# Kernel tuning notes

Measured on AMD Instinct MI355X. Metric: run time of the kernel, lower is better.

Reference implementation:

```python
import jax, jax.numpy as jnp
import numpy as np

B, N, C_IN, C_OUT, K, D_EMB = 32, 4096, 64, 64, 2, 16


def setup_inputs() -> dict:
    key = jax.random.key(0)
    ks = jax.random.split(key, 7)
    x = jax.random.normal(ks[0], (B, N, C_IN), jnp.float32)
    node_embeddings = jax.random.normal(ks[1], (N, D_EMB), jnp.float32)
    weights_pool = jax.random.normal(ks[2], (D_EMB, K, C_IN, C_OUT), jnp.float32) * 0.1
    bias_pool = jax.random.normal(ks[3], (D_EMB, C_OUT), jnp.float32) * 0.1
    lin_w = jax.random.normal(ks[4], (C_OUT, C_IN), jnp.float32) * 0.1
    lin_b = jax.random.normal(ks[5], (C_OUT,), jnp.float32) * 0.1
    adj = jax.random.uniform(ks[6], (N, N), jnp.float32)
    return dict(x=x, node_embeddings=node_embeddings, weights_pool=weights_pool,
                bias_pool=bias_pool, lin_w=lin_w, lin_b=lin_b, adj=adj)


def _sym_norm_adj(W):
    # W + 0.5*I, then D^{-1/2} W D^{-1/2} with D = diag(rowsum)
    n = W.shape[0]
    W = W + 0.5 * jnp.eye(n, dtype=W.dtype)
    sd = jnp.sqrt(1.0 / jnp.sum(W, axis=1))
    return sd[:, None] * W * sd[None, :]


def reference(x, node_embeddings, weights_pool, bias_pool, lin_w, lin_b, adj):
    n = node_embeddings.shape[0]
    # adaptive adjacency: softmax(relu(E E^T)) over neighbors
    supports_dyn = jax.nn.softmax(jax.nn.relu(node_embeddings @ node_embeddings.T), axis=1)
    supports = jnp.stack([jnp.eye(n, dtype=x.dtype), supports_dyn], axis=0)  # [K=2, N, N]
    # node-adaptive weights/bias generated from embeddings
    weights = jnp.einsum('nd,dkio->nkio', node_embeddings, weights_pool)  # [N,K,Cin,Cout]
    bias = node_embeddings @ bias_pool  # [N, Cout]
    # multi-hop aggregation + per-node conv
    x_g = jnp.einsum('knm,bmc->bnkc', supports, x)  # [B,N,K,Cin]
    x_gconv = jnp.einsum('bnki,nkio->bno', x_g, weights) + bias[None]  # [B,N,Cout]
    # static branch: init applies F.softmax(dim=1) to sym-normed adj, forward re-softmaxes dim=-1
    A = jax.nn.softmax(jax.nn.softmax(_sym_norm_adj(adj), axis=1), axis=-1)
    # einsum 'nm,bmc->bmc' == scale node m by sum_n A[n,m]
    scale = jnp.sum(A, axis=0)  # [N]
    x_static = (scale[None, :, None] * x) @ lin_w.T + lin_b  # [B,N,Cout]
    return x_gconv + jax.nn.sigmoid(x_static) * x_static
```

## Files before the change

### kernel.cpp

```cpp
#include <hip/hip_runtime.h>
#include <stdint.h>

#define Bdim 32
#define Ndim 4096
#define Cin  64
#define Cout 64
#define Demb 16

typedef __bf16 bf16x8 __attribute__((ext_vector_type(8)));
typedef float  f32x4  __attribute__((ext_vector_type(4)));

#define GLOBAL_AS(p) ((__attribute__((address_space(1))) void*)(p))
#define LDS_AS(p)    ((__attribute__((address_space(3))) void*)(p))
#define GLL(gp, lp)  __builtin_amdgcn_global_load_lds(GLOBAL_AS(gp), LDS_AS(lp), 16, 0, 0)

__device__ __forceinline__ uint16_t f2bf(float x) {
    union { float f; uint32_t u; } v; v.f = x;
    uint32_t r = v.u + 0x7FFFu + ((v.u >> 16) & 1u);
    return (uint16_t)(r >> 16);
}

__device__ __forceinline__ bf16x8 pack8(float4 a, float4 b) {
    union { uint16_t u[8]; bf16x8 v; } r;
    r.u[0] = f2bf(a.x); r.u[1] = f2bf(a.y); r.u[2] = f2bf(a.z); r.u[3] = f2bf(a.w);
    r.u[4] = f2bf(b.x); r.u[5] = f2bf(b.y); r.u[6] = f2bf(b.z); r.u[7] = f2bf(b.w);
    return r.v;
}

__global__ __launch_bounds__(256) void p1_prep(const float* __restrict__ E,
                                               const float* __restrict__ x,
                                               const float* __restrict__ adj,
                                               const float* __restrict__ pool,
                                               uint16_t* __restrict__ A,
                                               float* __restrict__ invA,
                                               uint16_t* __restrict__ Xtt,
                                               float* __restrict__ sd,
                                               float* __restrict__ scale,
                                               float* __restrict__ poolT) {
    __shared__ __align__(16) uint8_t smem[9232];
    const int t = threadIdx.x;
    const int blk = blockIdx.x;

    if (blk < 256) {
        float* Er_s = (float*)smem;
        float* red_s = (float*)(smem + 1024);
        const int n0 = blk * 16;
        Er_s[t] = E[n0 * Demb + t];
        __syncthreads();
        for (int half = 0; half < 2; ++half) {
            float er[8][16];
#pragma unroll
            for (int r = 0; r < 8; ++r)
#pragma unroll
                for (int d = 0; d < 16; ++d) er[r][d] = Er_s[(half * 8 + r) * 16 + d];
            float sacc[8];
#pragma unroll
            for (int r = 0; r < 8; ++r) sacc[r] = 0.f;
            for (int c = 0; c < 16; ++c) {
                const int m = c * 256 + t;
                const float4* ep = (const float4*)(E + (size_t)m * Demb);
                float4 e0 = ep[0], e1 = ep[1], e2 = ep[2], e3 = ep[3];
                float em[16] = {e0.x, e0.y, e0.z, e0.w, e1.x, e1.y, e1.z, e1.w,
                                e2.x, e2.y, e2.z, e2.w, e3.x, e3.y, e3.z, e3.w};
#pragma unroll
                for (int r = 0; r < 8; ++r) {
                    float v = 0.f;
#pragma unroll
                    for (int d = 0; d < 16; ++d) v = fmaf(er[r][d], em[d], v);
                    v = fmaxf(v, 0.f);
                    const float e = __expf(v);
                    sacc[r] += e;
                    A[(size_t)(n0 + half * 8 + r) * Ndim + m] = f2bf(e);
                }
            }
#pragma unroll
            for (int r = 0; r < 8; ++r) {
                float s = sacc[r];
#pragma unroll
                for (int off = 32; off > 0; off >>= 1) s += __shfl_down(s, off, 64);
                __syncthreads();
                if ((t & 63) == 0) red_s[t >> 6] = s;
                __syncthreads();
                if (t == 0)
                    invA[n0 + half * 8 + r] = 1.f / (red_s[0] + red_s[1] + red_s[2] + red_s[3]);
            }
            __syncthreads();
        }
    } else if (blk < 2304) {
        auto T = (uint16_t(*)[72])smem;
        const int idx = blk - 256;
        const int m0 = (idx & 63) * 64;
        const int b = idx >> 6;
        const int c = t & 63;
#pragma unroll
        for (int j = 0; j < 16; ++j) {
            const int m = (t >> 6) + j * 4;
            T[c][m] = f2bf(x[((size_t)b * Ndim + (m0 + m)) * Cin + c]);
        }
        __syncthreads();
        const int c2 = t >> 2, mo = (t & 3) * 16;
        const uint4* src = (const uint4*)&T[c2][mo];
        uint4 v0 = src[0], v1 = src[1];
        uint4* dst = (uint4*)(Xtt + (size_t)(b * Cin + c2) * Ndim + m0 + mo);
        dst[0] = v0;
        dst[1] = v1;
    } else if (blk < 6400) {
        float* red_s = (float*)smem;
        const int n = blk - 2304;
        if (n < 16) scale[n * 256 + t] = 0.f;
        const float4* ap = (const float4*)(adj + (size_t)n * Ndim);
        float s = 0.f;
#pragma unroll
        for (int q = 0; q < 4; ++q) {
            float4 a = ap[q * 256 + t];
            s += a.x + a.y + a.z + a.w;
        }
#pragma unroll
        for (int off = 32; off > 0; off >>= 1) s += __shfl_down(s, off, 64);
        if ((t & 63) == 0) red_s[t >> 6] = s;
        __syncthreads();
        if (t == 0) sd[n] = sqrtf(1.f / (red_s[0] + red_s[1] + red_s[2] + red_s[3] + 0.5f));
    } else {
        const int idx = blk - 6400;
        const int d = idx >> 2;
        const int base = (idx & 3) * 2048;
#pragma unroll
        for (int j = 0; j < 8; ++j) {
            const int e = base + j * 256 + t;
            const float v = pool[d * 8192 + e];
            poolT[d * 8192 + (e & 63) * 128 + (e >> 6)] = v;
        }
    }
}

__global__ __launch_bounds__(256) void p2_mid(const float* __restrict__ E,
                                              const float* __restrict__ adj,
                                              const float* __restrict__ sd,
                                              const float* __restrict__ poolT,
                                              const float* __restrict__ bias_pool,
                                              float* __restrict__ scale,
                                              uint16_t* __restrict__ Wt,
                                              float* __restrict__ biasn) {
    __shared__ __align__(16) uint8_t smem[16384];
    const int t = threadIdx.x;
    const int blk = blockIdx.x;

    if (blk < 256) {
        float* cs = (float*)smem;
#pragma unroll
        for (int i = 0; i < 16; ++i) cs[i * 256 + t] = 0.f;
        __syncthreads();

        const int wv = t >> 6, l = t & 63;
        const int nb = blk * 16 + wv * 4;

        float sdm[64];
#pragma unroll
        for (int i = 0; i < 16; ++i) {
            float4 s4 = *(const float4*)(sd + i * 256 + l * 4);
            sdm[i * 4 + 0] = s4.x; sdm[i * 4 + 1] = s4.y;
            sdm[i * 4 + 2] = s4.z; sdm[i * 4 + 3] = s4.w;
        }
        float colsum[64];
#pragma unroll
        for (int k = 0; k < 64; ++k) colsum[k] = 0.f;

        for (int r = 0; r < 4; ++r) {
            const int n = nb + r;
            const float sdn = sd[n];
            float e1[64];
            float s1 = 0.f;
#pragma unroll
            for (int i = 0; i < 16; ++i) {
                float4 a4 = *(const float4*)(adj + (size_t)n * Ndim + i * 256 + l * 4);
                const int c0 = i * 256 + l * 4;
                float vv[4] = {a4.x, a4.y, a4.z, a4.w};
#pragma unroll
                for (int u = 0; u < 4; ++u) {
                    const float vd = vv[u] + ((c0 + u) == n ? 0.5f : 0.f);
                    const float e = __expf(sdn * vd * sdm[i * 4 + u]);
                    e1[i * 4 + u] = e;
                    s1 += e;
                }
            }
#pragma unroll
            for (int off = 32; off > 0; off >>= 1) s1 += __shfl_xor(s1, off, 64);
            const float inv1 = 1.f / s1;
            float s2 = 0.f;
#pragma unroll
            for (int k = 0; k < 64; ++k) {
                const float e = __expf(e1[k] * inv1);
                e1[k] = e;
                s2 += e;
            }
#pragma unroll
            for (int off = 32; off > 0; off >>= 1) s2 += __shfl_xor(s2, off, 64);
            const float inv2 = 1.f / s2;
#pragma unroll
            for (int k = 0; k < 64; ++k) colsum[k] = fmaf(e1[k], inv2, colsum[k]);
        }
#pragma unroll
        for (int k = 0; k < 64; ++k)
            atomicAdd(&cs[(k >> 2) * 256 + l * 4 + (k & 3)], colsum[k]);
        __syncthreads();
#pragma unroll
        for (int i = 0; i < 16; ++i)
            atomicAdd(scale + i * 256 + t, cs[i * 256 + t]);
    } else {
        float* En = (float*)smem;
        const int idx = blk - 256;
        const int ec = idx & 7;
        const int n0 = (idx >> 3) * 32;
        En[t] = E[n0 * Demb + t];
        En[t + 256] = E[n0 * Demb + t + 256];
        __syncthreads();

        const int e0 = ec * 1024 + t * 4;
        float4 P[16];
#pragma unroll
        for (int d = 0; d < 16; ++d) P[d] = *(const float4*)(poolT + d * 8192 + e0);

        for (int g = 0; g < 32; ++g) {
            float4 acc = {0.f, 0.f, 0.f, 0.f};
#pragma unroll
            for (int d = 0; d < 16; ++d) {
                const float e = En[g * 16 + d];
                acc.x = fmaf(e, P[d].x, acc.x);
                acc.y = fmaf(e, P[d].y, acc.y);
                acc.z = fmaf(e, P[d].z, acc.z);
                acc.w = fmaf(e, P[d].w, acc.w);
            }
            union { uint16_t u[4]; uint2 v; } r;
            r.u[0] = f2bf(acc.x); r.u[1] = f2bf(acc.y);
            r.u[2] = f2bf(acc.z); r.u[3] = f2bf(acc.w);
            *(uint2*)(Wt + (size_t)(n0 + g) * 8192 + e0) = r.v;
        }

        if (ec == 0) {
            const int o = t & 63, gq = t >> 6;
#pragma unroll
            for (int gi = 0; gi < 8; ++gi) {
                const int g = gi * 4 + gq;
                float a = 0.f;
#pragma unroll
                for (int d = 0; d < 16; ++d) a = fmaf(En[g * 16 + d], bias_pool[d * 64 + o], a);
                biasn[(size_t)(n0 + g) * 64 + o] = a;
            }
        }
    }
}

#define GK 4096
#define GN 2048
#define K3_NT 64
__global__ __launch_bounds__(512) void k3_gemm(const uint16_t* __restrict__ Abf,
                                               const uint16_t* __restrict__ Bbf,
                                               const float* __restrict__ invA,
                                               uint16_t* __restrict__ Cbf) {
    __shared__ __align__(16) uint16_t As[3][256 * 64];
    __shared__ __align__(16) uint16_t Bs[3][128 * 64];
    const int t = threadIdx.x;
    const int lane = t & 63;
    const int wid = t >> 6;
    const int wr = wid >> 1;
    const int wc = wid & 1;

    const int bid = blockIdx.x;
    const int wgid = (bid & 7) * 32 + (bid >> 3);
    const int bm = (wgid >> 4) * 256;
    const int bn = (wgid & 15) * 128;

    const uint16_t* asrc[4];
    int adst[4];
#pragma unroll
    for (int i = 0; i < 4; ++i) {
        const int c = t + i * 512;
        const int row = c >> 3, ch = c & 7;
        asrc[i] = Abf + (size_t)(bm + row) * GK + ((ch ^ (row & 7)) << 3);
        adst[i] = c << 3;
    }
    const uint16_t* bsrc[2];
    int bdst[2];
#pragma unroll
    for (int i = 0; i < 2; ++i) {
        const int c = t + i * 512;
        const int row = c >> 3, ch = c & 7;
        bsrc[i] = Bbf + (size_t)(bn + row) * GK + ((ch ^ (row & 7)) << 3);
        bdst[i] = c << 3;
    }

    int offA[4][2], offB[4][2];
#pragma unroll
    for (int f = 0; f < 4; ++f)
#pragma unroll
        for (int ks = 0; ks < 2; ++ks) {
            const int ra = wr * 64 + f * 16 + (lane & 15);
            offA[f][ks] = ra * 64 + (((ks * 4 + (lane >> 4)) ^ (ra & 7)) << 3);
            const int rb = wc * 64 + f * 16 + (lane & 15);
            offB[f][ks] = rb * 64 + (((ks * 4 + (lane >> 4)) ^ (rb & 7)) << 3);
        }

    f32x4 acc[4][4];
#pragma unroll
    for (int i = 0; i < 4; ++i)
#pragma unroll
        for (int j = 0; j < 4; ++j) acc[i][j] = (f32x4){0.f, 0.f, 0.f, 0.f};

#define K3_STAGE(buf, kt)                                  \
    do {                                                   \
        const size_t ko_ = (size_t)(kt) * 64;              \
        GLL(asrc[0] + ko_, &As[buf][adst[0]]);             \
        GLL(asrc[1] + ko_, &As[buf][adst[1]]);             \
        GLL(asrc[2] + ko_, &As[buf][adst[2]]);             \
        GLL(asrc[3] + ko_, &As[buf][adst[3]]);             \
        GLL(bsrc[0] + ko_, &Bs[buf][bdst[0]]);             \
        GLL(bsrc[1] + ko_, &Bs[buf][bdst[1]]);             \
    } while (0)

    K3_STAGE(0, 0);
    K3_STAGE(1, 1);
    asm volatile("s_waitcnt vmcnt(6)" ::: "memory");
    __builtin_amdgcn_s_barrier();
    asm volatile("" ::: "memory");

    int cur = 0;
    for (int kt = 0; kt < K3_NT; ++kt) {
        if (kt < K3_NT - 2) {
            int nbuf = cur + 2; if (nbuf >= 3) nbuf -= 3;
            K3_STAGE(nbuf, kt + 2);
        }
        const uint16_t* Ab = As[cur];
        const uint16_t* Bb = Bs[cur];

        bf16x8 a0[4], b0[4];
#pragma unroll
        for (int f = 0; f < 4; ++f) a0[f] = *(const bf16x8*)(Ab + offA[f][0]);
#pragma unroll
        for (int j = 0; j < 4; ++j) b0[j] = *(const bf16x8*)(Bb + offB[j][0]);
        __builtin_amdgcn_s_setprio(1);
#pragma unroll
        for (int f = 0; f < 4; ++f)
#pragma unroll
            for (int j = 0; j < 4; ++j)
                acc[f][j] = __builtin_amdgcn_mfma_f32_16x16x32_bf16(a0[f], b0[j], acc[f][j], 0, 0, 0);
        __builtin_amdgcn_s_setprio(0);
        asm volatile("" ::: "memory");
        __builtin_amdgcn_s_barrier();
        asm volatile("" ::: "memory");

        bf16x8 a1[4], b1[4];
#pragma unroll
        for (int f = 0; f < 4; ++f) a1[f] = *(const bf16x8*)(Ab + offA[f][1]);
#pragma unroll
        for (int j = 0; j < 4; ++j) b1[j] = *(const bf16x8*)(Bb + offB[j][1]);
        __builtin_amdgcn_s_setprio(1);
#pragma unroll
        for (int f = 0; f < 4; ++f)
#pragma unroll
            for (int j = 0; j < 4; ++j)
                acc[f][j] = __builtin_amdgcn_mfma_f32_16x16x32_bf16(a1[f], b1[j], acc[f][j], 0, 0, 0);
        __builtin_amdgcn_s_setprio(0);

        if (kt < K3_NT - 2)
            asm volatile("s_waitcnt vmcnt(6)" ::: "memory");
        else
            asm volatile("s_waitcnt vmcnt(0)" ::: "memory");
        __builtin_amdgcn_s_barrier();
        asm volatile("" ::: "memory");

        if (++cur == 3) cur = 0;
    }
#undef K3_STAGE

#pragma unroll
    for (int f = 0; f < 4; ++f) {
        float invv[4];
#pragma unroll
        for (int r = 0; r < 4; ++r)
            invv[r] = invA[bm + wr * 64 + f * 16 + (lane >> 4) * 4 + r];
#pragma unroll
        for (int j = 0; j < 4; ++j)
#pragma unroll
            for (int r = 0; r < 4; ++r) {
                const int row = bm + wr * 64 + f * 16 + (lane >> 4) * 4 + r;
                const int col = bn + wc * 64 + j * 16 + (lane & 15);
                Cbf[(size_t)row * GN + col] = f2bf(acc[f][j][r] * invv[r]);
            }
    }
}

__global__ __launch_bounds__(256) void k6_gconv(const float* __restrict__ x,
                                                const uint16_t* __restrict__ XG,
                                                const uint16_t* __restrict__ Wt,
                                                const float* __restrict__ biasn,
                                                const float* __restrict__ scale,
                                                const float* __restrict__ lin_w,
                                                const float* __restrict__ lin_b,
                                                float* __restrict__ out) {
    __shared__ __align__(16) uint16_t Lws[64][72];
    const int t = threadIdx.x;
    const int n0 = blockIdx.x * 4;

    {
        const int o = t >> 2, i0 = (t & 3) * 16;
        const float4* lp = (const float4*)(lin_w + o * 64 + i0);
        float4 a0 = lp[0], a1 = lp[1], a2 = lp[2], a3 = lp[3];
        union { uint16_t u[16]; uint4 v[2]; } r;
        r.u[0] = f2bf(a0.x); r.u[1] = f2bf(a0.y); r.u[2]  = f2bf(a0.z); r.u[3]  = f2bf(a0.w);
        r.u[4] = f2bf(a1.x); r.u[5] = f2bf(a1.y); r.u[6]  = f2bf(a1.z); r.u[7]  = f2bf(a1.w);
        r.u[8] = f2bf(a2.x); r.u[9] = f2bf(a2.y); r.u[10] = f2bf(a2.z); r.u[11] = f2bf(a2.w);
        r.u[12] = f2bf(a3.x); r.u[13] = f2bf(a3.y); r.u[14] = f2bf(a3.z); r.u[15] = f2bf(a3.w);
        *(uint4*)&Lws[o][i0] = r.v[0];
        *(uint4*)&Lws[o][i0 + 8] = r.v[1];
    }

    const int w = t >> 6, lane = t & 63;
    const int n = n0 + w;
    const int l15 = lane & 15;
    const int q8 = (lane >> 4) * 8;

    bf16x8 a[2][4];
#pragma unroll
    for (int mt = 0; mt < 2; ++mt) {
        const int b = mt * 16 + l15;
        const float* xp = x + ((size_t)b * Ndim + n) * 64 + q8;
        a[mt][0] = pack8(((const float4*)xp)[0], ((const float4*)xp)[1]);
        a[mt][1] = pack8(((const float4*)(xp + 32))[0], ((const float4*)(xp + 32))[1]);
        const uint16_t* gp = XG + (size_t)n * 2048 + b * 64 + q8;
        a[mt][2] = *(const bf16x8*)gp;
        a[mt][3] = *(const bf16x8*)(gp + 32);
    }

    f32x4 accg[2][4], accs[2][4];
#pragma unroll
    for (int mt = 0; mt < 2; ++mt)
#pragma unroll
        for (int j = 0; j < 4; ++j) {
            accg[mt][j] = (f32x4){0.f, 0.f, 0.f, 0.f};
            accs[mt][j] = (f32x4){0.f, 0.f, 0.f, 0.f};
        }

    const uint16_t* wp = Wt + (size_t)n * 8192 + l15 * 128 + q8;

    __syncthreads();

#pragma unroll
    for (int ks = 0; ks < 4; ++ks) {
        bf16x8 bw[4];
#pragma unroll
        for (int j = 0; j < 4; ++j)
            bw[j] = *(const bf16x8*)(wp + j * 2048 + ks * 32);
#pragma unroll
        for (int mt = 0; mt < 2; ++mt)
#pragma unroll
            for (int j = 0; j < 4; ++j)
                accg[mt][j] = __builtin_amdgcn_mfma_f32_16x16x32_bf16(a[mt][ks], bw[j], accg[mt][j], 0, 0, 0);
        if (ks < 2) {
            bf16x8 bl[4];
#pragma unroll
            for (int j = 0; j < 4; ++j)
                bl[j] = *(const bf16x8*)&Lws[j * 16 + l15][ks * 32 + q8];
#pragma unroll
            for (int mt = 0; mt < 2; ++mt)
#pragma unroll
                for (int j = 0; j < 4; ++j)
                    accs[mt][j] = __builtin_amdgcn_mfma_f32_16x16x32_bf16(a[mt][ks], bl[j], accs[mt][j], 0, 0, 0);
        }
    }

    const float sc = scale[n];
#pragma unroll
    for (int j = 0; j < 4; ++j) {
        const int o = j * 16 + l15;
        const float bn = biasn[(size_t)n * 64 + o];
        const float lb = lin_b[o];
#pragma unroll
        for (int mt = 0; mt < 2; ++mt)
#pragma unroll
            for (int r = 0; r < 4; ++r) {
                const int b = mt * 16 + (lane >> 4) * 4 + r;
                const float gg = accg[mt][j][r] + bn;
                const float xs = sc * accs[mt][j][r] + lb;
                out[((size_t)b * Ndim + n) * 64 + o] = gg + xs / (1.f + __expf(-xs));
            }
    }
}

extern "C" void kernel_launch(void* const* d_in, const int* in_sizes, int n_in,
                              void* d_out, int out_size, void* d_ws, size_t ws_size,
                              hipStream_t stream) {
    const float* x         = (const float*)d_in[0];
    const float* E         = (const float*)d_in[1];
    const float* pool      = (const float*)d_in[2];
    const float* bias_pool = (const float*)d_in[3];
    const float* lin_w     = (const float*)d_in[4];
    const float* lin_b     = (const float*)d_in[5];
    const float* adj       = (const float*)d_in[6];
    float* out = (float*)d_out;

    uint8_t* ws = (uint8_t*)d_ws;
    uint16_t* A     = (uint16_t*)(ws);
    uint16_t* Xtt   = (uint16_t*)(ws + 33554432);
    uint16_t* XG    = (uint16_t*)(ws + 50331648);
    uint16_t* Wt    = (uint16_t*)(ws + 67108864);
    float*    biasn = (float*)   (ws + 134217728);
    float*    sd    = (float*)   (ws + 135266304);
    float*    scale = (float*)   (ws + 135282688);
    float*    poolT = (float*)   (ws + 135299072);
    float*    invA  = (float*)   (ws + 135823360);

    p1_prep<<<dim3(6464), dim3(256), 0, stream>>>(E, x, adj, pool, A, invA, Xtt, sd, scale, poolT);
    p2_mid<<<dim3(1280), dim3(256), 0, stream>>>(E, adj, sd, poolT, bias_pool, scale, Wt, biasn);
    k3_gemm<<<dim3(256), dim3(512), 0, stream>>>(A, Xtt, invA, XG);
    k6_gconv<<<dim3(1024), dim3(256), 0, stream>>>(x, XG, Wt, biasn, scale, lin_w, lin_b, out);
}
```

Baseline: 351.0 us.

## Shrink k3 GEMM tile to 128x128 with 256 threads and double buffering

Changes the dense GEMM from 256x128 tiles on 512-thread blocks with a 3-stage LDS pipeline to 128x128 tiles on 256-thread blocks with a 2-stage pipeline, launching 512 blocks instead of 256. Both k-substeps' fragments are loaded at once and each iteration ends with a single __syncthreads. This cuts LDS use per block and doubles the block count so more workgroups can be resident. In exchange, each block reuses less data, so global traffic for A and B rises, and prefetch depth is lower with coarser synchronisation.

```diff
diff --git a/kernel.cpp b/kernel.cpp
--- a/kernel.cpp
+++ b/kernel.cpp
@@ -253,12 +253,12 @@
 #define GK 4096
 #define GN 2048
 #define K3_NT 64
-__global__ __launch_bounds__(512) void k3_gemm(const uint16_t* __restrict__ Abf,
+__global__ __launch_bounds__(256) void k3_gemm(const uint16_t* __restrict__ Abf,
                                                const uint16_t* __restrict__ Bbf,
                                                const float* __restrict__ invA,
                                                uint16_t* __restrict__ Cbf) {
-    __shared__ __align__(16) uint16_t As[3][256 * 64];
-    __shared__ __align__(16) uint16_t Bs[3][128 * 64];
+    __shared__ __align__(16) uint16_t As[2][128 * 64];
+    __shared__ __align__(16) uint16_t Bs[2][128 * 64];
     const int t = threadIdx.x;
     const int lane = t & 63;
     const int wid = t >> 6;
@@ -266,27 +266,20 @@
     const int wc = wid & 1;
 
     const int bid = blockIdx.x;
-    const int wgid = (bid & 7) * 32 + (bid >> 3);
-    const int bm = (wgid >> 4) * 256;
+    const int wgid = (bid & 7) * 64 + (bid >> 3);
+    const int bm = (wgid >> 4) * 128;
     const int bn = (wgid & 15) * 128;
 
     const uint16_t* asrc[4];
-    int adst[4];
+    const uint16_t* bsrc[4];
+    int cdst[4];
 #pragma unroll
     for (int i = 0; i < 4; ++i) {
-        const int c = t + i * 512;
+        const int c = t + i * 256;
         const int row = c >> 3, ch = c & 7;
         asrc[i] = Abf + (size_t)(bm + row) * GK + ((ch ^ (row & 7)) << 3);
-        adst[i] = c << 3;
-    }
-    const uint16_t* bsrc[2];
-    int bdst[2];
-#pragma unroll
-    for (int i = 0; i < 2; ++i) {
-        const int c = t + i * 512;
-        const int row = c >> 3, ch = c & 7;
         bsrc[i] = Bbf + (size_t)(bn + row) * GK + ((ch ^ (row & 7)) << 3);
-        bdst[i] = c << 3;
+        cdst[i] = c << 3;
     }
 
     int offA[4][2], offB[4][2];
@@ -309,66 +302,43 @@
 #define K3_STAGE(buf, kt)                                  \
     do {                                                   \
         const size_t ko_ = (size_t)(kt) * 64;              \
-        GLL(asrc[0] + ko_, &As[buf][adst[0]]);             \
-        GLL(asrc[1] + ko_, &As[buf][adst[1]]);             \
-        GLL(asrc[2] + ko_, &As[buf][adst[2]]);             \
-        GLL(asrc[3] + ko_, &As[buf][adst[3]]);             \
-        GLL(bsrc[0] + ko_, &Bs[buf][bdst[0]]);             \
-        GLL(bsrc[1] + ko_, &Bs[buf][bdst[1]]);             \
+        GLL(asrc[0] + ko_, &As[buf][cdst[0]]);             \
+        GLL(asrc[1] + ko_, &As[buf][cdst[1]]);             \
+        GLL(asrc[2] + ko_, &As[buf][cdst[2]]);             \
+        GLL(asrc[3] + ko_, &As[buf][cdst[3]]);             \
+        GLL(bsrc[0] + ko_, &Bs[buf][cdst[0]]);             \
+        GLL(bsrc[1] + ko_, &Bs[buf][cdst[1]]);             \
+        GLL(bsrc[2] + ko_, &Bs[buf][cdst[2]]);             \
+        GLL(bsrc[3] + ko_, &Bs[buf][cdst[3]]);             \
     } while (0)
 
     K3_STAGE(0, 0);
-    K3_STAGE(1, 1);
-    asm volatile("s_waitcnt vmcnt(6)" ::: "memory");
-    __builtin_amdgcn_s_barrier();
-    asm volatile("" ::: "memory");
-
-    int cur = 0;
+    __syncthreads();
+
     for (int kt = 0; kt < K3_NT; ++kt) {
-        if (kt < K3_NT - 2) {
-            int nbuf = cur + 2; if (nbuf >= 3) nbuf -= 3;
-            K3_STAGE(nbuf, kt + 2);
-        }
+        const int cur = kt & 1;
+        if (kt < K3_NT - 1) K3_STAGE(cur ^ 1, kt + 1);
+
         const uint16_t* Ab = As[cur];
         const uint16_t* Bb = Bs[cur];
-
-        bf16x8 a0[4], b0[4];
-#pragma unroll
-        for (int f = 0; f < 4; ++f) a0[f] = *(const bf16x8*)(Ab + offA[f][0]);
-#pragma unroll
-        for (int j = 0; j < 4; ++j) b0[j] = *(const bf16x8*)(Bb + offB[j][0]);
+        bf16x8 af[4][2], bfr[4][2];
+#pragma unroll
+        for (int ks = 0; ks < 2; ++ks) {
+#pragma unroll
+            for (int f = 0; f < 4; ++f) af[f][ks] = *(const bf16x8*)(Ab + offA[f][ks]);
+#pragma unroll
+            for (int j = 0; j < 4; ++j) bfr[j][ks] = *(const bf16x8*)(Bb + offB[j][ks]);
+        }
         __builtin_amdgcn_s_setprio(1);
 #pragma unroll
-        for (int f = 0; f < 4; ++f)
-#pragma unroll
-            for (int j = 0; j < 4; ++j)
-                acc[f][j] = __builtin_amdgcn_mfma_f32_16x16x32_bf16(a0[f], b0[j], acc[f][j], 0, 0, 0);
+        for (int ks = 0; ks < 2; ++ks)
+#pragma unroll
+            for (int f = 0; f < 4; ++f)
+#pragma unroll
+                for (int j = 0; j < 4; ++j)
+                    acc[f][j] = __builtin_amdgcn_mfma_f32_16x16x32_bf16(af[f][ks], bfr[j][ks], acc[f][j], 0, 0, 0);
         __builtin_amdgcn_s_setprio(0);
-        asm volatile("" ::: "memory");
-        __builtin_amdgcn_s_barrier();
-        asm volatile("" ::: "memory");
-
-        bf16x8 a1[4], b1[4];
-#pragma unroll
-        for (int f = 0; f < 4; ++f) a1[f] = *(const bf16x8*)(Ab + offA[f][1]);
-#pragma unroll
-        for (int j = 0; j < 4; ++j) b1[j] = *(const bf16x8*)(Bb + offB[j][1]);
-        __builtin_amdgcn_s_setprio(1);
-#pragma unroll
-        for (int f = 0; f < 4; ++f)
-#pragma unroll
-            for (int j = 0; j < 4; ++j)
-                acc[f][j] = __builtin_amdgcn_mfma_f32_16x16x32_bf16(a1[f], b1[j], acc[f][j], 0, 0, 0);
-        __builtin_amdgcn_s_setprio(0);
-
-        if (kt < K3_NT - 2)
-            asm volatile("s_waitcnt vmcnt(6)" ::: "memory");
-        else
-            asm volatile("s_waitcnt vmcnt(0)" ::: "memory");
-        __builtin_amdgcn_s_barrier();
-        asm volatile("" ::: "memory");
-
-        if (++cur == 3) cur = 0;
+        __syncthreads();
     }
 #undef K3_STAGE
 
@@ -511,6 +481,6 @@
 
     p1_prep<<<dim3(6464), dim3(256), 0, stream>>>(E, x, adj, pool, A, invA, Xtt, sd, scale, poolT);
     p2_mid<<<dim3(1280), dim3(256), 0, stream>>>(E, adj, sd, poolT, bias_pool, scale, Wt, biasn);
-    k3_gemm<<<dim3(256), dim3(512), 0, stream>>>(A, Xtt, invA, XG);
+    k3_gemm<<<dim3(512), dim3(256), 0, stream>>>(A, Xtt, invA, XG);
     k6_gconv<<<dim3(1024), dim3(256), 0, stream>>>(x, XG, Wt, biasn, scale, lin_w, lin_b, out);
 }
```

New measurement: 336.2 us. -4.2%, faster.
